# Kernel optimization log

Measured on AMD Instinct MI355X. Metric: run time of the kernel, lower is better.

## Reference

```python
import jax, jax.numpy as jnp
import numpy as np

D_MODEL = 768
N_HEADS = 12
D_HEAD = 64
D_EMBED = N_HEADS * D_HEAD  # 768


def setup_inputs() -> dict:
    key = jax.random.key(0)
    ks = jax.random.split(key, 5)
    b, p = 2, 2048
    x = jax.random.normal(ks[0], (b, p, D_MODEL), dtype=jnp.float32)
    # nn.Linear default init scale ~ 1/sqrt(fan_in)
    Wqkv = jax.random.normal(ks[1], (D_MODEL, 3 * D_EMBED), dtype=jnp.float32) / np.sqrt(D_MODEL)
    bqkv = jax.random.normal(ks[2], (3 * D_EMBED,), dtype=jnp.float32) * 0.01
    Wout = jax.random.normal(ks[3], (D_EMBED, D_MODEL), dtype=jnp.float32) / np.sqrt(D_EMBED)
    bout = jax.random.normal(ks[4], (D_MODEL,), dtype=jnp.float32) * 0.01
    return {"x": x, "Wqkv": Wqkv, "bqkv": bqkv, "Wout": Wout, "bout": bout}


def reference(x, Wqkv, bqkv, Wout, bout):
    b, p, d = x.shape
    qkv = x @ Wqkv + bqkv                                   # [b, p, 3*D_EMBED]
    qkv = qkv.reshape(b, p, N_HEADS, 3 * D_HEAD).transpose(0, 2, 1, 3)  # [b, h, p, 3*dh]
    q, k, v = jnp.split(qkv, 3, axis=-1)                    # each [b, h, p, dh]
    # FAITHFUL to source bug: logits /= d_head**(-0.5)  ==  logits *= sqrt(d_head)
    logits = jnp.einsum('bhqd,bhkd->bhqk', q, k) * jnp.sqrt(jnp.float32(D_HEAD))
    attn = jax.nn.softmax(logits, axis=-1)                  # [b, h, p, p]
    out = jnp.einsum('bhqk,bhkd->bhqd', attn, v)            # [b, h, p, dh]
    out = out.transpose(0, 2, 1, 3).reshape(b, p, D_EMBED)  # [b, p, D_EMBED]
    return out @ Wout + bout                                # [b, p, D_MODEL]
```

## Files before the change

### kernel.cpp

```cpp
#include <hip/hip_runtime.h>
#include <stdint.h>

#define LOG2E 1.44269504088896340736f

typedef __bf16 v8bf __attribute__((ext_vector_type(8)));
typedef _Float16 v8h __attribute__((ext_vector_type(8)));
typedef float f32x4 __attribute__((ext_vector_type(4)));
typedef float f32x16 __attribute__((ext_vector_type(16)));
typedef unsigned int v4u __attribute__((ext_vector_type(4)));
typedef unsigned int v2u __attribute__((ext_vector_type(2)));

__device__ __forceinline__ unsigned short f2bf(float f) {
  union { float f; uint32_t u; } v; v.f = f;
  uint32_t u = v.u;
  uint32_t r = (u + 0x7FFFu + ((u >> 16) & 1u)) >> 16;
  return (unsigned short)r;
}
__device__ __forceinline__ void gll16(const void* g, void* l) {
  __builtin_amdgcn_global_load_lds(
      (const __attribute__((address_space(1))) unsigned int*)g,
      (__attribute__((address_space(3))) unsigned int*)l, 16, 0, 0);
}
__device__ __forceinline__ uint32_t pk2(float a, float b) {
  union { __bf16 h[2]; uint32_t u; } x;
  x.h[0] = (__bf16)a; x.h[1] = (__bf16)b;
  return x.u;
}


__global__ void prep_fused(const float* __restrict__ x, const float* __restrict__ Wqkv,
                           const float* __restrict__ Wout,
                           _Float16* __restrict__ Ah,
                           _Float16* __restrict__ Whk,
                           _Float16* __restrict__ Wv,
                           unsigned short* __restrict__ WoT) {
  const int t = threadIdx.x, f = blockIdx.x;
  if (f < 12288) {
    int m = f / 3, n = (f - m * 3) * 256 + t;
    Ah[(size_t)m * 768 + n] = (_Float16)x[(size_t)m * 768 + n];
  } else if (f < 19200) {
    int g = f - 12288;
    int cp = g / 3, k = (g - cp * 3) * 256 + t;
    int n;
    if (cp < 1536) n = (cp >> 7) * 192 + (cp & 127);
    else           n = ((cp - 1536) >> 6) * 192 + 128 + ((cp - 1536) & 63);
    float v = Wqkv[(size_t)k * 2304 + n];
    if (cp < 1536) Whk[(size_t)cp * 768 + k] = (_Float16)v;
    else           Wv[(size_t)(cp - 1536) * 768 + k] = (_Float16)v;
  } else {
    int g = f - 19200;
    int n = g / 3, k = (g - n * 3) * 256 + t;
    WoT[(size_t)n * 768 + k] = f2bf(Wout[(size_t)k * 768 + n]);
  }
}

__global__ __launch_bounds__(256) void gemm_qkv(
    const _Float16* __restrict__ Ah, const _Float16* __restrict__ Whk,
    const _Float16* __restrict__ Wv, const float* __restrict__ bqkv,
    _Float16* __restrict__ Qh, _Float16* __restrict__ Kh,
    unsigned short* __restrict__ VT) {
  __shared__ _Float16 As[128 * 32];
  __shared__ _Float16 Bs[128 * 32];
  const int t = threadIdx.x, f = blockIdx.x;
  const int w = t >> 6, l = t & 63, lr = l & 15, lg = l >> 4;
  const int wm = (w >> 1) * 64, wn = (w & 1) * 64;
  f32x4 acc[4][4] = {};

  if (f < 384) {
    const int xcd = f & 7, s = f >> 3;
    const int m0 = (xcd * 4 + (s & 3)) * 128;
    const int xt = s >> 2;
    const _Float16* Ap = Ah + (size_t)m0 * 768;
    const _Float16* Bp = Whk + (size_t)xt * 128 * 768;
    for (int kt = 0; kt < 24; ++kt) {
      const int k0 = kt << 5;
      const int c0 = t, c1 = t + 256;
      gll16(Ap + (size_t)(c0 >> 2) * 768 + k0 + ((c0 & 3) << 3), &As[c0 * 8]);
      gll16(Ap + (size_t)(c1 >> 2) * 768 + k0 + ((c1 & 3) << 3), &As[c1 * 8]);
      gll16(Bp + (size_t)(c0 >> 2) * 768 + k0 + ((c0 & 3) << 3), &Bs[c0 * 8]);
      gll16(Bp + (size_t)(c1 >> 2) * 768 + k0 + ((c1 & 3) << 3), &Bs[c1 * 8]);
      __syncthreads();
      v8h a[4], b[4];
#pragma unroll
      for (int i = 0; i < 4; i++) {
        a[i] = *(const v8h*)&As[(wm + i * 16 + lr) * 32 + lg * 8];
        b[i] = *(const v8h*)&Bs[(wn + i * 16 + lr) * 32 + lg * 8];
      }
#pragma unroll
      for (int i = 0; i < 4; i++)
#pragma unroll
        for (int j = 0; j < 4; j++)
          acc[i][j] = __builtin_amdgcn_mfma_f32_16x16x32_f16(a[i], b[j], acc[i][j], 0, 0, 0);
      __syncthreads();
    }
#pragma unroll
    for (int j = 0; j < 4; j++) {
      const int jj = j * 16 + lr;
      const float bv = bqkv[xt * 192 + wn + jj];
#pragma unroll
      for (int i = 0; i < 4; i++) {
#pragma unroll
        for (int r = 0; r < 4; r++) {
          const int m = m0 + wm + i * 16 + lg * 4 + r;
          const int b = m >> 11, p = m & 2047;
          size_t base = ((size_t)(b * 12 + xt) * 2048 + p) * 64;
          float val = acc[i][j][r] + bv;
          if (wn == 0) Qh[base + jj] = (_Float16)(val * (8.0f * LOG2E));
          else         Kh[base + jj] = (_Float16)val;
        }
      }
    }
  } else {
    const int g = f - 384;
    const int xcd = g & 7, s = g >> 3;
    const int m0v = (xcd * 4 + (s & 3)) * 128;
    const int d0 = (s >> 2) * 128;
    for (int kt = 0; kt < 24; ++kt) {
      const int k0 = kt << 5;
      const int c0 = t, c1 = t + 256;
      gll16(Wv + (size_t)(d0 + (c0 >> 2)) * 768 + k0 + ((c0 & 3) << 3), &As[c0 * 8]);
      gll16(Wv + (size_t)(d0 + (c1 >> 2)) * 768 + k0 + ((c1 & 3) << 3), &As[c1 * 8]);
      gll16(Ah + (size_t)(m0v + (c0 >> 2)) * 768 + k0 + ((c0 & 3) << 3), &Bs[c0 * 8]);
      gll16(Ah + (size_t)(m0v + (c1 >> 2)) * 768 + k0 + ((c1 & 3) << 3), &Bs[c1 * 8]);
      __syncthreads();
      v8h a[4], b[4];
#pragma unroll
      for (int i = 0; i < 4; i++) {
        a[i] = *(const v8h*)&As[(wm + i * 16 + lr) * 32 + lg * 8];
        b[i] = *(const v8h*)&Bs[(wn + i * 16 + lr) * 32 + lg * 8];
      }
#pragma unroll
      for (int i = 0; i < 4; i++)
#pragma unroll
        for (int j = 0; j < 4; j++)
          acc[i][j] = __builtin_amdgcn_mfma_f32_16x16x32_f16(a[i], b[j], acc[i][j], 0, 0, 0);
      __syncthreads();
    }
#pragma unroll
    for (int i = 0; i < 4; i++) {
#pragma unroll
      for (int r = 0; r < 4; r++) {
        const int drow = d0 + wm + i * 16 + lg * 4 + r;
        const int h = drow >> 6, dd = drow & 63;
        const float bv = bqkv[h * 192 + 128 + dd];
#pragma unroll
        for (int j = 0; j < 4; j++) {
          const int m = m0v + wn + j * 16 + lr;
          const int b = m >> 11, p = m & 2047;
          VT[((size_t)(b * 12 + h) * 64 + dd) * 2048 + p] = f2bf(acc[i][j][r] + bv);
        }
      }
    }
  }
}

__global__ __launch_bounds__(256) void gemm_out(
    const unsigned short* __restrict__ A, const unsigned short* __restrict__ B,
    const float* __restrict__ bias, float* __restrict__ C) {
  __shared__ unsigned short As[64 * 32];
  __shared__ unsigned short Bs[128 * 32];
  const int t = threadIdx.x, f = blockIdx.x;
  const int xcd = f & 7, s = f >> 3;
  const int m0 = (xcd * 8 + (s & 7)) * 64;
  const int n0 = (s >> 3) * 128;
  const int w = t >> 6, l = t & 63, lr = l & 15, lg = l >> 4;
  const int wm = (w >> 1) * 32, wn = (w & 1) * 64;
  f32x4 acc[2][4] = {};
  for (int kt = 0; kt < 24; ++kt) {
    const int k0 = kt << 5;
    gll16(A + (size_t)(m0 + (t >> 2)) * 768 + k0 + ((t & 3) << 3), &As[t * 8]);
    gll16(B + (size_t)(n0 + (t >> 2)) * 768 + k0 + ((t & 3) << 3), &Bs[t * 8]);
    gll16(B + (size_t)(n0 + 64 + (t >> 2)) * 768 + k0 + ((t & 3) << 3), &Bs[(t + 256) * 8]);
    __syncthreads();
    v8bf a[2], b[4];
#pragma unroll
    for (int i = 0; i < 2; i++)
      a[i] = *(const v8bf*)&As[(wm + i * 16 + lr) * 32 + lg * 8];
#pragma unroll
    for (int j = 0; j < 4; j++)
      b[j] = *(const v8bf*)&Bs[(wn + j * 16 + lr) * 32 + lg * 8];
#pragma unroll
    for (int i = 0; i < 2; i++)
#pragma unroll
      for (int j = 0; j < 4; j++)
        acc[i][j] = __builtin_amdgcn_mfma_f32_16x16x32_bf16(a[i], b[j], acc[i][j], 0, 0, 0);
    __syncthreads();
  }
#pragma unroll
  for (int i = 0; i < 2; i++) {
#pragma unroll
    for (int j = 0; j < 4; j++) {
      const int col = n0 + wn + j * 16 + lr;
      const float bv = bias[col];
#pragma unroll
      for (int r = 0; r < 4; r++) {
        const int row = m0 + wm + i * 16 + lg * 4 + r;
        C[(size_t)row * 768 + col] = acc[i][j][r] + bv;
      }
    }
  }
}

__global__ __launch_bounds__(256, 3) void attn(
    const _Float16* __restrict__ Qh, const _Float16* __restrict__ Kh,
    const unsigned short* __restrict__ VT,
    float* __restrict__ Op, float* __restrict__ Ml) {
  __shared__ __align__(16) _Float16 Ks[2][32 * 64];
  __shared__ __align__(16) unsigned short Vs[2][64 * 32];
  __shared__ float Al[4][32];
  const int t = threadIdx.x, w = t >> 6, l = t & 63;
  const int lq = l & 31, hi = l >> 5;
  const int f = blockIdx.x;
  const int xcd = f & 7, slot = f >> 3;
  const int p = xcd + 8 * (slot >> 4);
  const int bh = p >> 1, zsplit = p & 1;
  const int q0 = (slot & 15) * 128;
  const int qw0 = q0 + w * 32;
  const int NKT = 32;
  const int ktBase = zsplit * 32;
  const _Float16* Qb = Qh + (size_t)bh * 2048 * 64;
  const _Float16* Kb = Kh + (size_t)bh * 2048 * 64;
  const unsigned short* Vb = VT + (size_t)bh * 64 * 2048;

  const int krow = t >> 3, kpart = t & 7;
  const int kwofs = (krow * 64 + kpart * 8) ^ ((krow & 7) << 3);
  const int vd = t >> 2, vpart = t & 3;
  const int vwofs = (vd * 32 + vpart * 8) ^ ((vd & 3) << 3);

  const char* gK = (const char*)Kb + (size_t)ktBase * 4096 + (size_t)t * 16;
  const char* gV = (const char*)Vb + (size_t)vd * 4096 + (size_t)vpart * 16
                   + (size_t)ktBase * 64;

  v4u kreg, vreg;
  kreg = *(const v4u*)gK;
  vreg = *(const v4u*)gV;
  *(v4u*)&Ks[0][kwofs] = kreg;
  *(v4u*)&Vs[0][vwofs] = vreg;
  gK += 4096; gV += 64;
  kreg = *(const v4u*)gK;
  vreg = *(const v4u*)gV;

  v8h qf[4];
#pragma unroll
  for (int ks = 0; ks < 4; ++ks)
    qf[ks] = *(const v8h*)(Qb + (size_t)(qw0 + lq) * 64 + ks * 16 + hi * 8);

  f32x16 o0 = {}, o1 = {};
  float mrun = -1e30f, lsum = 0.f;
  const int sxk = (lq & 7) << 3;
  const int sxv = (lq & 3) << 3;
  __syncthreads();

  for (int kt = 0; kt < NKT; ++kt) {
    const _Float16* ksb = &Ks[kt & 1][0];
    const unsigned short* vsb = &Vs[kt & 1][0];
    _Float16* ksw = &Ks[(kt & 1) ^ 1][0];
    unsigned short* vsw = &Vs[(kt & 1) ^ 1][0];

    f32x16 s = {};
    __builtin_amdgcn_s_setprio(1);
#pragma unroll
    for (int ks = 0; ks < 4; ++ks) {
      v8h ka = *(const v8h*)&ksb[(lq * 64 + ks * 16 + hi * 8) ^ sxk];
      s = __builtin_amdgcn_mfma_f32_32x32x16_f16(ka, qf[ks], s, 0, 0, 0);
    }
    __builtin_amdgcn_s_setprio(0);

    if (kt < NKT - 1) {
      *(v4u*)&ksw[kwofs] = kreg;
      *(v4u*)&vsw[vwofs] = vreg;
    }
    if (kt < NKT - 2) {
      gK += 4096; gV += 64;
      kreg = *(const v4u*)gK;
      vreg = *(const v4u*)gV;
    }

    float tm[8];
#pragma unroll
    for (int i = 0; i < 8; i++) tm[i] = fmaxf(s[i], s[i + 8]);
#pragma unroll
    for (int i = 0; i < 4; i++) tm[i] = fmaxf(tm[i], tm[i + 4]);
    float pmax = fmaxf(fmaxf(tm[0], tm[1]), fmaxf(tm[2], tm[3]));
    {
      v2u r = __builtin_amdgcn_permlane32_swap(__float_as_uint(pmax),
                                               __float_as_uint(pmax), false, false);
      pmax = fmaxf(__uint_as_float(r.x), __uint_as_float(r.y));
    }

    if (__any(pmax > mrun + 32.f)) {
      float mnew = fmaxf(mrun, pmax);
      float a = __builtin_exp2f(mrun - mnew);
      mrun = mnew;
      lsum *= a;
      if (!hi) Al[w][lq] = a;
#pragma unroll
      for (int r = 0; r < 16; r++) {
        float ar = Al[w][(r & 3) + 8 * (r >> 2) + 4 * hi];
        o0[r] *= ar; o1[r] *= ar;
      }
    }

#pragma unroll
    for (int i = 0; i < 16; i++) s[i] = __builtin_exp2f(s[i] - mrun);
    {
      float a0 = (s[0] + s[8]) + (s[1] + s[9]);
      float a1 = (s[2] + s[10]) + (s[3] + s[11]);
      float a2 = (s[4] + s[12]) + (s[5] + s[13]);
      float a3 = (s[6] + s[14]) + (s[7] + s[15]);
      float ps = (a0 + a1) + (a2 + a3);
      v2u r = __builtin_amdgcn_permlane32_swap(__float_as_uint(ps),
                                               __float_as_uint(ps), false, false);
      lsum += __uint_as_float(r.x) + __uint_as_float(r.y);
    }
    uint32_t paw[2][4];
    {
      v2u r0 = __builtin_amdgcn_permlane32_swap(pk2(s[0], s[1]), pk2(s[4], s[5]), false, false);
      v2u r1 = __builtin_amdgcn_permlane32_swap(pk2(s[2], s[3]), pk2(s[6], s[7]), false, false);
      paw[0][0] = r0.x; paw[0][2] = r0.y; paw[0][1] = r1.x; paw[0][3] = r1.y;
      v2u r2 = __builtin_amdgcn_permlane32_swap(pk2(s[8], s[9]), pk2(s[12], s[13]), false, false);
      v2u r3 = __builtin_amdgcn_permlane32_swap(pk2(s[10], s[11]), pk2(s[14], s[15]), false, false);
      paw[1][0] = r2.x; paw[1][2] = r2.y; paw[1][1] = r3.x; paw[1][3] = r3.y;
    }

    __builtin_amdgcn_s_setprio(1);
#pragma unroll
    for (int ks = 0; ks < 2; ++ks) {
      union { uint32_t u[4]; v8bf v; } pa;
      pa.u[0] = paw[ks][0]; pa.u[1] = paw[ks][1];
      pa.u[2] = paw[ks][2]; pa.u[3] = paw[ks][3];
      v8bf v0 = *(const v8bf*)&vsb[(lq * 32 + ks * 16 + hi * 8) ^ sxv];
      v8bf v1 = *(const v8bf*)&vsb[((lq + 32) * 32 + ks * 16 + hi * 8) ^ sxv];
      o0 = __builtin_amdgcn_mfma_f32_32x32x16_bf16(pa.v, v0, o0, 0, 0, 0);
      o1 = __builtin_amdgcn_mfma_f32_32x32x16_bf16(pa.v, v1, o1, 0, 0, 0);
    }
    __builtin_amdgcn_s_setprio(0);
    if (kt < NKT - 1) __syncthreads();
  }

  const size_t S = (size_t)24 * 2048;
  const size_t srow = (size_t)zsplit * S + (size_t)bh * 2048;
  if (!hi) {
    Ml[(srow + qw0 + lq) * 2]     = mrun;
    Ml[(srow + qw0 + lq) * 2 + 1] = lsum;
  }
#pragma unroll
  for (int r = 0; r < 16; r++) {
    const int q = qw0 + (r & 3) + 8 * (r >> 2) + 4 * hi;
    Op[(srow + q) * 64 + lq]      = o0[r];
    Op[(srow + q) * 64 + 32 + lq] = o1[r];
  }
}

__global__ __launch_bounds__(256) void attn_combine(
    const float* __restrict__ Op, const float* __restrict__ Ml,
    __bf16* __restrict__ Oe) {
  const size_t S = (size_t)24 * 2048;
  int row = blockIdx.x * 4 + (threadIdx.x >> 6);
  int lane = threadIdx.x & 63;
  int bh = row >> 11, q = row & 2047;
  int b = bh / 12, h = bh - b * 12;
  float m1 = Ml[(size_t)row * 2], l1 = Ml[(size_t)row * 2 + 1];
  float m2 = Ml[(S + row) * 2],   l2 = Ml[(S + row) * 2 + 1];
  float M = fmaxf(m1, m2);
  float a1 = __builtin_exp2f(m1 - M);
  float a2 = __builtin_exp2f(m2 - M);
  float rinv = 1.0f / (l1 * a1 + l2 * a2);
  float o1 = Op[(size_t)row * 64 + lane];
  float o2 = Op[S * 64 + (size_t)row * 64 + lane];
  Oe[((size_t)(b * 2048 + q)) * 768 + h * 64 + lane] = (__bf16)((o1 * a1 + o2 * a2) * rinv);
}

extern "C" void kernel_launch(void* const* d_in, const int* in_sizes, int n_in,
                              void* d_out, int out_size, void* d_ws, size_t ws_size,
                              hipStream_t stream) {
  const float* x    = (const float*)d_in[0];
  const float* Wqkv = (const float*)d_in[1];
  const float* bqkv = (const float*)d_in[2];
  const float* Wout = (const float*)d_in[3];
  const float* bout = (const float*)d_in[4];
  float* out = (float*)d_out;
  char* ws = (char*)d_ws;

  _Float16*       Ah    = (_Float16*)(ws + 0);
  _Float16*       Whk   = (_Float16*)(ws + 18874368);
  _Float16*       Wv    = (_Float16*)(ws + 25952256);
  _Float16*       Qh    = (_Float16*)(ws + 67239936);
  _Float16*       Kh    = (_Float16*)(ws + 86114304);
  unsigned short* VT    = (unsigned short*)(ws + 104988672);
  unsigned short* Oemb  = (unsigned short*)(ws + 111280128);
  unsigned short* WoT   = (unsigned short*)(ws + 117571584);
  float*          Opart = (float*)(ws + 0);
  float*          Mlpart= (float*)(ws + 50331648);

  prep_fused<<<dim3(21504), 256, 0, stream>>>(x, Wqkv, Wout, Ah, Whk, Wv, WoT);
  gemm_qkv<<<dim3(576), 256, 0, stream>>>(Ah, Whk, Wv, bqkv, Qh, Kh, VT);
  attn<<<dim3(768), 256, 0, stream>>>(Qh, Kh, VT, Opart, Mlpart);
  attn_combine<<<dim3(12288), 256, 0, stream>>>(Opart, Mlpart, (__bf16*)Oemb);
  gemm_out<<<dim3(384), 256, 0, stream>>>(Oemb, WoT, bout, out);
}
```

Baseline: 138.9 us.

## Split attention KV into four chunks with 64-key tiles and higher occupancy

The attention kernel's KV split grows from two to four partitions, which doubles the grid. Each iteration now processes a 64-key tile with two score MFMAs and four PV MFMAs, and the occupancy hint rises from 3 to 4 blocks per CU. The combine kernel merges four partial (m, l, O) sets instead of two, and the Ml buffer offset moves so it does not overlap the larger partial-output buffer. The aim is more parallelism and fewer loop iterations and barriers per key. The cost is twice the partial-output traffic in the combine pass and more register pressure, which may cause spills under the tighter launch bound.

```diff
diff --git a/kernel.cpp b/kernel.cpp
--- a/kernel.cpp
+++ b/kernel.cpp
@@ -201,44 +201,57 @@
   }
 }
 
-__global__ __launch_bounds__(256, 3) void attn(
+__global__ __launch_bounds__(256, 4) void attn(
     const _Float16* __restrict__ Qh, const _Float16* __restrict__ Kh,
     const unsigned short* __restrict__ VT,
     float* __restrict__ Op, float* __restrict__ Ml) {
-  __shared__ __align__(16) _Float16 Ks[2][32 * 64];
-  __shared__ __align__(16) unsigned short Vs[2][64 * 32];
+  __shared__ __align__(16) _Float16 Ks[2][64 * 64];
+  __shared__ __align__(16) unsigned short Vs[2][64 * 64];
   __shared__ float Al[4][32];
   const int t = threadIdx.x, w = t >> 6, l = t & 63;
   const int lq = l & 31, hi = l >> 5;
   const int f = blockIdx.x;
   const int xcd = f & 7, slot = f >> 3;
   const int p = xcd + 8 * (slot >> 4);
-  const int bh = p >> 1, zsplit = p & 1;
+  const int bh = p >> 2, zsplit = p & 3;
   const int q0 = (slot & 15) * 128;
   const int qw0 = q0 + w * 32;
-  const int NKT = 32;
-  const int ktBase = zsplit * 32;
+  const int NKT = 8;
+  const int ktBase = zsplit * 8;
   const _Float16* Qb = Qh + (size_t)bh * 2048 * 64;
   const _Float16* Kb = Kh + (size_t)bh * 2048 * 64;
   const unsigned short* Vb = VT + (size_t)bh * 64 * 2048;
 
-  const int krow = t >> 3, kpart = t & 7;
-  const int kwofs = (krow * 64 + kpart * 8) ^ ((krow & 7) << 3);
-  const int vd = t >> 2, vpart = t & 3;
-  const int vwofs = (vd * 32 + vpart * 8) ^ ((vd & 3) << 3);
-
-  const char* gK = (const char*)Kb + (size_t)ktBase * 4096 + (size_t)t * 16;
-  const char* gV = (const char*)Vb + (size_t)vd * 4096 + (size_t)vpart * 16
-                   + (size_t)ktBase * 64;
-
-  v4u kreg, vreg;
-  kreg = *(const v4u*)gK;
-  vreg = *(const v4u*)gV;
-  *(v4u*)&Ks[0][kwofs] = kreg;
-  *(v4u*)&Vs[0][vwofs] = vreg;
-  gK += 4096; gV += 64;
-  kreg = *(const v4u*)gK;
-  vreg = *(const v4u*)gV;
+  int kwofs[2], vwofs[2];
+#pragma unroll
+  for (int i = 0; i < 2; i++) {
+    int c = t + i * 256;
+    int row = c >> 3, part = c & 7;
+    kwofs[i] = (row * 64 + part * 8) ^ ((row & 7) << 3);
+    vwofs[i] = kwofs[i];
+  }
+
+  const char* gK = (const char*)Kb + (size_t)ktBase * 8192 + (size_t)t * 16;
+  const char* gV = (const char*)Vb + (size_t)(t >> 3) * 4096 + (size_t)(t & 7) * 16
+                   + (size_t)ktBase * 128;
+
+  v4u kreg[2], vreg[2];
+#pragma unroll
+  for (int i = 0; i < 2; i++) {
+    kreg[i] = *(const v4u*)(gK + i * 4096);
+    vreg[i] = *(const v4u*)(gV + i * 131072);
+  }
+#pragma unroll
+  for (int i = 0; i < 2; i++) {
+    *(v4u*)&Ks[0][kwofs[i]] = kreg[i];
+    *(v4u*)&Vs[0][vwofs[i]] = vreg[i];
+  }
+  gK += 8192; gV += 128;
+#pragma unroll
+  for (int i = 0; i < 2; i++) {
+    kreg[i] = *(const v4u*)(gK + i * 4096);
+    vreg[i] = *(const v4u*)(gV + i * 131072);
+  }
 
   v8h qf[4];
 #pragma unroll
@@ -247,8 +260,7 @@
 
   f32x16 o0 = {}, o1 = {};
   float mrun = -1e30f, lsum = 0.f;
-  const int sxk = (lq & 7) << 3;
-  const int sxv = (lq & 3) << 3;
+  const int sx = (lq & 7) << 3;
   __syncthreads();
 
   for (int kt = 0; kt < NKT; ++kt) {
@@ -257,28 +269,38 @@
     _Float16* ksw = &Ks[(kt & 1) ^ 1][0];
     unsigned short* vsw = &Vs[(kt & 1) ^ 1][0];
 
-    f32x16 s = {};
+    f32x16 s0 = {}, s1 = {};
     __builtin_amdgcn_s_setprio(1);
 #pragma unroll
     for (int ks = 0; ks < 4; ++ks) {
-      v8h ka = *(const v8h*)&ksb[(lq * 64 + ks * 16 + hi * 8) ^ sxk];
-      s = __builtin_amdgcn_mfma_f32_32x32x16_f16(ka, qf[ks], s, 0, 0, 0);
+      v8h ka = *(const v8h*)&ksb[((lq) * 64 + ks * 16 + hi * 8) ^ sx];
+      v8h kb = *(const v8h*)&ksb[((lq + 32) * 64 + ks * 16 + hi * 8) ^ sx];
+      s0 = __builtin_amdgcn_mfma_f32_32x32x16_f16(ka, qf[ks], s0, 0, 0, 0);
+      s1 = __builtin_amdgcn_mfma_f32_32x32x16_f16(kb, qf[ks], s1, 0, 0, 0);
     }
     __builtin_amdgcn_s_setprio(0);
 
     if (kt < NKT - 1) {
-      *(v4u*)&ksw[kwofs] = kreg;
-      *(v4u*)&vsw[vwofs] = vreg;
+#pragma unroll
+      for (int i = 0; i < 2; i++) {
+        *(v4u*)&ksw[kwofs[i]] = kreg[i];
+        *(v4u*)&vsw[vwofs[i]] = vreg[i];
+      }
     }
     if (kt < NKT - 2) {
-      gK += 4096; gV += 64;
-      kreg = *(const v4u*)gK;
-      vreg = *(const v4u*)gV;
-    }
-
-    float tm[8];
-#pragma unroll
-    for (int i = 0; i < 8; i++) tm[i] = fmaxf(s[i], s[i + 8]);
+      gK += 8192; gV += 128;
+#pragma unroll
+      for (int i = 0; i < 2; i++) {
+        kreg[i] = *(const v4u*)(gK + i * 4096);
+        vreg[i] = *(const v4u*)(gV + i * 131072);
+      }
+    }
+
+    float tm[16];
+#pragma unroll
+    for (int i = 0; i < 16; i++) tm[i] = fmaxf(s0[i], s1[i]);
+#pragma unroll
+    for (int i = 0; i < 8; i++) tm[i] = fmaxf(tm[i], tm[i + 8]);
 #pragma unroll
     for (int i = 0; i < 4; i++) tm[i] = fmaxf(tm[i], tm[i + 4]);
     float pmax = fmaxf(fmaxf(tm[0], tm[1]), fmaxf(tm[2], tm[3]));
@@ -302,35 +324,43 @@
     }
 
 #pragma unroll
-    for (int i = 0; i < 16; i++) s[i] = __builtin_exp2f(s[i] - mrun);
+    for (int i = 0; i < 16; i++) s0[i] = __builtin_exp2f(s0[i] - mrun);
+#pragma unroll
+    for (int i = 0; i < 16; i++) s1[i] = __builtin_exp2f(s1[i] - mrun);
     {
-      float a0 = (s[0] + s[8]) + (s[1] + s[9]);
-      float a1 = (s[2] + s[10]) + (s[3] + s[11]);
-      float a2 = (s[4] + s[12]) + (s[5] + s[13]);
-      float a3 = (s[6] + s[14]) + (s[7] + s[15]);
+      float a0 = (s0[0] + s0[8]) + (s0[1] + s0[9]) + (s1[0] + s1[8]) + (s1[1] + s1[9]);
+      float a1 = (s0[2] + s0[10]) + (s0[3] + s0[11]) + (s1[2] + s1[10]) + (s1[3] + s1[11]);
+      float a2 = (s0[4] + s0[12]) + (s0[5] + s0[13]) + (s1[4] + s1[12]) + (s1[5] + s1[13]);
+      float a3 = (s0[6] + s0[14]) + (s0[7] + s0[15]) + (s1[6] + s1[14]) + (s1[7] + s1[15]);
       float ps = (a0 + a1) + (a2 + a3);
       v2u r = __builtin_amdgcn_permlane32_swap(__float_as_uint(ps),
                                                __float_as_uint(ps), false, false);
       lsum += __uint_as_float(r.x) + __uint_as_float(r.y);
     }
-    uint32_t paw[2][4];
+    uint32_t paw[4][4];
     {
-      v2u r0 = __builtin_amdgcn_permlane32_swap(pk2(s[0], s[1]), pk2(s[4], s[5]), false, false);
-      v2u r1 = __builtin_amdgcn_permlane32_swap(pk2(s[2], s[3]), pk2(s[6], s[7]), false, false);
+      v2u r0 = __builtin_amdgcn_permlane32_swap(pk2(s0[0], s0[1]), pk2(s0[4], s0[5]), false, false);
+      v2u r1 = __builtin_amdgcn_permlane32_swap(pk2(s0[2], s0[3]), pk2(s0[6], s0[7]), false, false);
       paw[0][0] = r0.x; paw[0][2] = r0.y; paw[0][1] = r1.x; paw[0][3] = r1.y;
-      v2u r2 = __builtin_amdgcn_permlane32_swap(pk2(s[8], s[9]), pk2(s[12], s[13]), false, false);
-      v2u r3 = __builtin_amdgcn_permlane32_swap(pk2(s[10], s[11]), pk2(s[14], s[15]), false, false);
+      v2u r2 = __builtin_amdgcn_permlane32_swap(pk2(s0[8], s0[9]), pk2(s0[12], s0[13]), false, false);
+      v2u r3 = __builtin_amdgcn_permlane32_swap(pk2(s0[10], s0[11]), pk2(s0[14], s0[15]), false, false);
       paw[1][0] = r2.x; paw[1][2] = r2.y; paw[1][1] = r3.x; paw[1][3] = r3.y;
+      v2u r4 = __builtin_amdgcn_permlane32_swap(pk2(s1[0], s1[1]), pk2(s1[4], s1[5]), false, false);
+      v2u r5 = __builtin_amdgcn_permlane32_swap(pk2(s1[2], s1[3]), pk2(s1[6], s1[7]), false, false);
+      paw[2][0] = r4.x; paw[2][2] = r4.y; paw[2][1] = r5.x; paw[2][3] = r5.y;
+      v2u r6 = __builtin_amdgcn_permlane32_swap(pk2(s1[8], s1[9]), pk2(s1[12], s1[13]), false, false);
+      v2u r7 = __builtin_amdgcn_permlane32_swap(pk2(s1[10], s1[11]), pk2(s1[14], s1[15]), false, false);
+      paw[3][0] = r6.x; paw[3][2] = r6.y; paw[3][1] = r7.x; paw[3][3] = r7.y;
     }
 
     __builtin_amdgcn_s_setprio(1);
 #pragma unroll
-    for (int ks = 0; ks < 2; ++ks) {
+    for (int ks = 0; ks < 4; ++ks) {
       union { uint32_t u[4]; v8bf v; } pa;
       pa.u[0] = paw[ks][0]; pa.u[1] = paw[ks][1];
       pa.u[2] = paw[ks][2]; pa.u[3] = paw[ks][3];
-      v8bf v0 = *(const v8bf*)&vsb[(lq * 32 + ks * 16 + hi * 8) ^ sxv];
-      v8bf v1 = *(const v8bf*)&vsb[((lq + 32) * 32 + ks * 16 + hi * 8) ^ sxv];
+      v8bf v0 = *(const v8bf*)&vsb[((lq) * 64 + ks * 16 + hi * 8) ^ sx];
+      v8bf v1 = *(const v8bf*)&vsb[((lq + 32) * 64 + ks * 16 + hi * 8) ^ sx];
       o0 = __builtin_amdgcn_mfma_f32_32x32x16_bf16(pa.v, v0, o0, 0, 0, 0);
       o1 = __builtin_amdgcn_mfma_f32_32x32x16_bf16(pa.v, v1, o1, 0, 0, 0);
     }
@@ -360,15 +390,21 @@
   int lane = threadIdx.x & 63;
   int bh = row >> 11, q = row & 2047;
   int b = bh / 12, h = bh - b * 12;
-  float m1 = Ml[(size_t)row * 2], l1 = Ml[(size_t)row * 2 + 1];
-  float m2 = Ml[(S + row) * 2],   l2 = Ml[(S + row) * 2 + 1];
-  float M = fmaxf(m1, m2);
-  float a1 = __builtin_exp2f(m1 - M);
-  float a2 = __builtin_exp2f(m2 - M);
-  float rinv = 1.0f / (l1 * a1 + l2 * a2);
-  float o1 = Op[(size_t)row * 64 + lane];
-  float o2 = Op[S * 64 + (size_t)row * 64 + lane];
-  Oe[((size_t)(b * 2048 + q)) * 768 + h * 64 + lane] = (__bf16)((o1 * a1 + o2 * a2) * rinv);
+  float m[4], lv[4];
+#pragma unroll
+  for (int s = 0; s < 4; s++) {
+    m[s]  = Ml[(s * S + row) * 2];
+    lv[s] = Ml[(s * S + row) * 2 + 1];
+  }
+  float M = fmaxf(fmaxf(m[0], m[1]), fmaxf(m[2], m[3]));
+  float num = 0.f, den = 0.f;
+#pragma unroll
+  for (int s = 0; s < 4; s++) {
+    float a = __builtin_exp2f(m[s] - M);
+    den += lv[s] * a;
+    num += Op[(s * S + row) * 64 + lane] * a;
+  }
+  Oe[((size_t)(b * 2048 + q)) * 768 + h * 64 + lane] = (__bf16)(num / den);
 }
 
 extern "C" void kernel_launch(void* const* d_in, const int* in_sizes, int n_in,
@@ -391,11 +427,11 @@
   unsigned short* Oemb  = (unsigned short*)(ws + 111280128);
   unsigned short* WoT   = (unsigned short*)(ws + 117571584);
   float*          Opart = (float*)(ws + 0);
-  float*          Mlpart= (float*)(ws + 50331648);
+  float*          Mlpart= (float*)(ws + 52428800);
 
   prep_fused<<<dim3(21504), 256, 0, stream>>>(x, Wqkv, Wout, Ah, Whk, Wv, WoT);
   gemm_qkv<<<dim3(576), 256, 0, stream>>>(Ah, Whk, Wv, bqkv, Qh, Kh, VT);
-  attn<<<dim3(768), 256, 0, stream>>>(Qh, Kh, VT, Opart, Mlpart);
+  attn<<<dim3(1536), 256, 0, stream>>>(Qh, Kh, VT, Opart, Mlpart);
   attn_combine<<<dim3(12288), 256, 0, stream>>>(Opart, Mlpart, (__bf16*)Oemb);
   gemm_out<<<dim3(384), 256, 0, stream>>>(Oemb, WoT, bout, out);
 }
```

Result: slower. 143.4 us (+3.2%).

## Split attention KV range four ways and store partial outputs in bf16

Applied to the files above, without the earlier changes.

The attention kernel now splits each (batch, head) key range into four chunks instead of two, launching twice as many blocks that each do half as many KV tiles. The combine kernel merges four partial results using their per-row max and sum statistics. Partial outputs are stored as bf16 rather than fp32, and launch bounds now target four blocks per CU. The aim is more parallelism and less partial-output traffic, at the cost of a larger combine step, a possible tail wave, and reduced precision in the unnormalised partials.

```diff
diff --git a/kernel.cpp b/kernel.cpp
--- a/kernel.cpp
+++ b/kernel.cpp
@@ -201,10 +201,10 @@
   }
 }
 
-__global__ __launch_bounds__(256, 3) void attn(
+__global__ __launch_bounds__(256, 4) void attn(
     const _Float16* __restrict__ Qh, const _Float16* __restrict__ Kh,
     const unsigned short* __restrict__ VT,
-    float* __restrict__ Op, float* __restrict__ Ml) {
+    __bf16* __restrict__ Op, float* __restrict__ Ml) {
   __shared__ __align__(16) _Float16 Ks[2][32 * 64];
   __shared__ __align__(16) unsigned short Vs[2][64 * 32];
   __shared__ float Al[4][32];
@@ -213,11 +213,11 @@
   const int f = blockIdx.x;
   const int xcd = f & 7, slot = f >> 3;
   const int p = xcd + 8 * (slot >> 4);
-  const int bh = p >> 1, zsplit = p & 1;
+  const int bh = p >> 2, zsplit = p & 3;
   const int q0 = (slot & 15) * 128;
   const int qw0 = q0 + w * 32;
-  const int NKT = 32;
-  const int ktBase = zsplit * 32;
+  const int NKT = 16;
+  const int ktBase = zsplit * 16;
   const _Float16* Qb = Qh + (size_t)bh * 2048 * 64;
   const _Float16* Kb = Kh + (size_t)bh * 2048 * 64;
   const unsigned short* Vb = VT + (size_t)bh * 64 * 2048;
@@ -347,28 +347,34 @@
 #pragma unroll
   for (int r = 0; r < 16; r++) {
     const int q = qw0 + (r & 3) + 8 * (r >> 2) + 4 * hi;
-    Op[(srow + q) * 64 + lq]      = o0[r];
-    Op[(srow + q) * 64 + 32 + lq] = o1[r];
+    Op[(srow + q) * 64 + lq]      = (__bf16)o0[r];
+    Op[(srow + q) * 64 + 32 + lq] = (__bf16)o1[r];
   }
 }
 
 __global__ __launch_bounds__(256) void attn_combine(
-    const float* __restrict__ Op, const float* __restrict__ Ml,
+    const __bf16* __restrict__ Op, const float* __restrict__ Ml,
     __bf16* __restrict__ Oe) {
   const size_t S = (size_t)24 * 2048;
   int row = blockIdx.x * 4 + (threadIdx.x >> 6);
   int lane = threadIdx.x & 63;
   int bh = row >> 11, q = row & 2047;
   int b = bh / 12, h = bh - b * 12;
-  float m1 = Ml[(size_t)row * 2], l1 = Ml[(size_t)row * 2 + 1];
-  float m2 = Ml[(S + row) * 2],   l2 = Ml[(S + row) * 2 + 1];
-  float M = fmaxf(m1, m2);
-  float a1 = __builtin_exp2f(m1 - M);
-  float a2 = __builtin_exp2f(m2 - M);
-  float rinv = 1.0f / (l1 * a1 + l2 * a2);
-  float o1 = Op[(size_t)row * 64 + lane];
-  float o2 = Op[S * 64 + (size_t)row * 64 + lane];
-  Oe[((size_t)(b * 2048 + q)) * 768 + h * 64 + lane] = (__bf16)((o1 * a1 + o2 * a2) * rinv);
+  float m[4], lv[4];
+#pragma unroll
+  for (int s = 0; s < 4; s++) {
+    m[s]  = Ml[(s * S + row) * 2];
+    lv[s] = Ml[(s * S + row) * 2 + 1];
+  }
+  float M = fmaxf(fmaxf(m[0], m[1]), fmaxf(m[2], m[3]));
+  float num = 0.f, den = 0.f;
+#pragma unroll
+  for (int s = 0; s < 4; s++) {
+    float a = __builtin_exp2f(m[s] - M);
+    den += lv[s] * a;
+    num += (float)Op[(s * S + row) * 64 + lane] * a;
+  }
+  Oe[((size_t)(b * 2048 + q)) * 768 + h * 64 + lane] = (__bf16)(num / den);
 }
 
 extern "C" void kernel_launch(void* const* d_in, const int* in_sizes, int n_in,
@@ -390,12 +396,12 @@
   unsigned short* VT    = (unsigned short*)(ws + 104988672);
   unsigned short* Oemb  = (unsigned short*)(ws + 111280128);
   unsigned short* WoT   = (unsigned short*)(ws + 117571584);
-  float*          Opart = (float*)(ws + 0);
-  float*          Mlpart= (float*)(ws + 50331648);
+  __bf16*         Opart = (__bf16*)(ws + 0);
+  float*          Mlpart= (float*)(ws + 52428800);
 
   prep_fused<<<dim3(21504), 256, 0, stream>>>(x, Wqkv, Wout, Ah, Whk, Wv, WoT);
   gemm_qkv<<<dim3(576), 256, 0, stream>>>(Ah, Whk, Wv, bqkv, Qh, Kh, VT);
-  attn<<<dim3(768), 256, 0, stream>>>(Qh, Kh, VT, Opart, Mlpart);
+  attn<<<dim3(1536), 256, 0, stream>>>(Qh, Kh, VT, Opart, Mlpart);
   attn_combine<<<dim3(12288), 256, 0, stream>>>(Opart, Mlpart, (__bf16*)Oemb);
   gemm_out<<<dim3(384), 256, 0, stream>>>(Oemb, WoT, bout, out);
 }
```

Result: no change. 137.2 us (median of 2 runs) (-1.2%).
